# Kernel optimization log

Hardware: AMD Instinct MI355X
Metric: run time of the kernel (lower is better)

## Reference

```python
import jax, jax.numpy as jnp
import numpy as np

B, K = 2048, 256
ED = RD = HD = 256
AD = ED + RD          # action_dim = 512
IN = ED + HD + RD     # 768
NUM_E, NUM_R = 100000, 500
HUGE = jnp.float32(1e31)  # ops.HUGE_INT


def setup_inputs() -> dict:
    key = jax.random.key(0)
    ks = jax.random.split(key, 12)
    s = 0.05  # keep logits in a sane range
    E = jax.random.normal(ks[0], (B, ED), jnp.float32)
    H = jax.random.normal(ks[1], (B, HD), jnp.float32)
    Q = jax.random.normal(ks[2], (B, RD), jnp.float32)
    W1 = jax.random.normal(ks[3], (AD, IN), jnp.float32) * s
    b1 = jnp.zeros((AD,), jnp.float32)
    W2 = jax.random.normal(ks[4], (AD, AD), jnp.float32) * s
    b2 = jnp.zeros((AD,), jnp.float32)
    emb_r = jax.random.normal(ks[5], (NUM_R, RD), jnp.float32) * s
    emb_e = jax.random.normal(ks[6], (NUM_E, ED), jnp.float32) * s
    # binary action mask (variable-size action spaces, padded); col 0 always valid
    action_mask = (jax.random.uniform(ks[7], (B, K)) > 0.3).astype(jnp.float32)
    action_mask = action_mask.at[:, 0].set(1.0)
    r_space = jax.random.randint(ks[8], (B, K), 0, NUM_R)
    e_space = jax.random.randint(ks[9], (B, K), 0, NUM_E)
    return {"E": E, "H": H, "Q": Q, "W1": W1, "b1": b1, "W2": W2, "b2": b2,
            "emb_r": emb_r, "emb_e": emb_e, "action_mask": action_mask,
            "r_space": r_space, "e_space": e_space}


def reference(E, H, Q, W1, b1, W2, b2, emb_r, emb_e, action_mask, r_space, e_space):
    # state MLP: X = W2Dropout(W2(relu(W1(cat([E, H, Q])))))  (dropout = identity at eval)
    X = jnp.concatenate([E, H, Q], axis=-1)           # [B, IN]
    X = jax.nn.relu(X @ W1.T + b1)                    # [B, AD]
    X2 = X @ W2.T + b2                                # [B, AD]
    # gather action embeddings: A = cat([emb_r[r], emb_e[e]])  [B, K, AD]
    A = jnp.concatenate([emb_r[r_space], emb_e[e_space]], axis=-1)
    # masked softmax over action space
    scores = jnp.einsum('bkd,bd->bk', A, X2) - (1.0 - action_mask) * HUGE
    action_dist = jax.nn.softmax(scores, axis=-1)     # [B, K]
    entropy = -jnp.sum(action_dist * jnp.log(action_dist + 1e-20), axis=-1)  # [B]
    return action_dist, entropy
```

## Files before the change

kernel.cpp:

```cpp
#include <hip/hip_runtime.h>
#include <hip/hip_bf16.h>
#include <hip/hip_fp8.h>
#include <math.h>

#define B_   2048
#define K_   256
#define AD_  512
#define IN_  768
#define NR_  500
#define NRP_ 512
#define NE_  100000

typedef __attribute__((ext_vector_type(8))) short short8;
typedef __attribute__((ext_vector_type(4))) float float4v;
typedef __attribute__((ext_vector_type(4))) float f32x4;

__device__ __forceinline__ unsigned short f2bf(float f) {
    unsigned int u = __float_as_uint(f);
    unsigned int r = u + 0x7FFF + ((u >> 16) & 1);
    return (unsigned short)(r >> 16);
}
__device__ __forceinline__ float bf2f(short s) {
    return __uint_as_float(((unsigned int)(unsigned short)s) << 16);
}
__device__ __forceinline__ unsigned char f2fp8(float f) {
    __hip_fp8_e4m3 t(f);
    return (unsigned char)t.__x;
}
__device__ __forceinline__ float fp8tof(unsigned int byte) {
    __hip_fp8_e4m3 t; t.__x = (__hip_fp8_storage_t)byte; return (float)t;
}
__device__ __forceinline__ float dot4_fp8(unsigned int d, const float* x) {
    return fp8tof(d & 0xffu)         * x[0] + fp8tof((d >> 8) & 0xffu)  * x[1]
         + fp8tof((d >> 16) & 0xffu) * x[2] + fp8tof(d >> 24)           * x[3];
}

#define X_N4  (B_ * IN_ / 4)
#define W1_N4 (AD_ * IN_ / 4)
#define W2_N4 (AD_ * AD_ / 4)
#define ER_N4 (NR_ * 256 / 4)
#define PREPS_TOTAL (X_N4 + W1_N4 + W2_N4 + ER_N4)
__global__ __launch_bounds__(256) void prep_small_kernel(
    const float* __restrict__ E, const float* __restrict__ H,
    const float* __restrict__ Q, const float* __restrict__ W1,
    const float* __restrict__ W2, const float* __restrict__ emb_r,
    ushort* __restrict__ Xb, ushort* __restrict__ W1b,
    ushort* __restrict__ W2b, ushort* __restrict__ emb_rb)
{
    int t = blockIdx.x * 256 + threadIdx.x;
    const float* src; ushort* dst; long off;
    if (t < X_N4) {
        const int base = t * 4;
        const int row = base / IN_, col = base % IN_;
        src = (col < 256) ? &E[row * 256 + col]
            : (col < 512) ? &H[row * 256 + col - 256]
                          : &Q[row * 256 + col - 512];
        const float4 v = *(const float4*)src;
        ushort4 o;
        o.x = f2bf(v.x); o.y = f2bf(v.y); o.z = f2bf(v.z); o.w = f2bf(v.w);
        *(ushort4*)&Xb[base] = o;
        return;
    }
    t -= X_N4;
    if (t < W1_N4)                 { src = W1;    dst = W1b;    off = t; }
    else if (t < W1_N4 + W2_N4)    { src = W2;    dst = W2b;    off = t - W1_N4; }
    else if (t < W1_N4 + W2_N4 + ER_N4) { src = emb_r; dst = emb_rb; off = t - W1_N4 - W2_N4; }
    else return;
    const float4 v = *(const float4*)&src[off * 4];
    ushort4 o;
    o.x = f2bf(v.x); o.y = f2bf(v.y); o.z = f2bf(v.z); o.w = f2bf(v.w);
    *(ushort4*)&dst[off * 4] = o;
}

#define EE_N4 (NE_ * 256 / 4)
__device__ __forceinline__ void conv_range(
    const float* __restrict__ emb_e, unsigned char* __restrict__ emb_e8,
    int q0, int q1, int cb)
{
    const int stride = 256 * 256;
    const f32x4* __restrict__ src = (const f32x4*)emb_e;
    uchar4* __restrict__ dst = (uchar4*)emb_e8;
    int i = q0 + cb * 256 + (int)threadIdx.x;
    for (; i + 3 * stride < q1; i += 4 * stride) {
        f32x4 v0 = __builtin_nontemporal_load(src + i);
        f32x4 v1 = __builtin_nontemporal_load(src + i + stride);
        f32x4 v2 = __builtin_nontemporal_load(src + i + 2 * stride);
        f32x4 v3 = __builtin_nontemporal_load(src + i + 3 * stride);
        uchar4 o0, o1, o2, o3;
        o0.x = f2fp8(v0[0]); o0.y = f2fp8(v0[1]); o0.z = f2fp8(v0[2]); o0.w = f2fp8(v0[3]);
        o1.x = f2fp8(v1[0]); o1.y = f2fp8(v1[1]); o1.z = f2fp8(v1[2]); o1.w = f2fp8(v1[3]);
        o2.x = f2fp8(v2[0]); o2.y = f2fp8(v2[1]); o2.z = f2fp8(v2[2]); o2.w = f2fp8(v2[3]);
        o3.x = f2fp8(v3[0]); o3.y = f2fp8(v3[1]); o3.z = f2fp8(v3[2]); o3.w = f2fp8(v3[3]);
        dst[i] = o0; dst[i + stride] = o1; dst[i + 2 * stride] = o2; dst[i + 3 * stride] = o3;
    }
    for (; i < q1; i += stride) {
        f32x4 v = __builtin_nontemporal_load(src + i);
        uchar4 o;
        o.x = f2fp8(v[0]); o.y = f2fp8(v[1]); o.z = f2fp8(v[2]); o.w = f2fp8(v[3]);
        dst[i] = o;
    }
}

template<int K, bool RELU, bool OUT_BF16, bool BIAS, bool EMIT_RHALF>
__global__ __launch_bounds__(256) void gemm_bf16_kernel(
    const ushort* __restrict__ A, const ushort* __restrict__ Bw,
    const float* __restrict__ bias, ushort* __restrict__ outb,
    float* __restrict__ outf, ushort* __restrict__ rhalf,
    const float* __restrict__ emb_e, unsigned char* __restrict__ emb_e8,
    int q0, int q1)
{
    constexpr int PITCH = 72;
    __shared__ ushort Asl[2][64 * PITCH];
    __shared__ ushort Bsl[2][64 * PITCH];

    if (blockIdx.x >= 8) {
        conv_range(emb_e, emb_e8, q0, q1, (int)(blockIdx.x - 8) * 32 + (int)blockIdx.y);
        return;
    }

    const int tid = threadIdx.x;
    const int lane = tid & 63, w = tid >> 6;
    const int n0 = blockIdx.x * 64, m0 = blockIdx.y * 64;
    const int lrow = tid >> 2, lcg = (tid & 3) * 16;
    const int q = lane >> 4, l16 = lane & 15;

    const ushort* aptr = &A[(size_t)(m0 + lrow) * K + lcg];
    const ushort* bptr = &Bw[(size_t)(n0 + lrow) * K + lcg];

    short8 ra0 = *(const short8*)aptr;
    short8 ra1 = *(const short8*)(aptr + 8);
    short8 rb0 = *(const short8*)bptr;
    short8 rb1 = *(const short8*)(bptr + 8);
    *(short8*)&Asl[0][lrow * PITCH + lcg]     = ra0;
    *(short8*)&Asl[0][lrow * PITCH + lcg + 8] = ra1;
    *(short8*)&Bsl[0][lrow * PITCH + lcg]     = rb0;
    *(short8*)&Bsl[0][lrow * PITCH + lcg + 8] = rb1;

    float4v acc[4] = {};
    int buf = 0;
    __syncthreads();
    for (int k0 = 0; k0 < K; k0 += 64) {
        if (k0 + 64 < K) {
            ra0 = *(const short8*)(aptr + k0 + 64);
            ra1 = *(const short8*)(aptr + k0 + 64 + 8);
            rb0 = *(const short8*)(bptr + k0 + 64);
            rb1 = *(const short8*)(bptr + k0 + 64 + 8);
        }
        #pragma unroll
        for (int kh = 0; kh < 64; kh += 32) {
            const short8 af = *(const short8*)&Asl[buf][(w * 16 + l16) * PITCH + kh + q * 8];
            #pragma unroll
            for (int jn = 0; jn < 4; ++jn) {
                const short8 bfr = *(const short8*)&Bsl[buf][(jn * 16 + l16) * PITCH + kh + q * 8];
                acc[jn] = __builtin_amdgcn_mfma_f32_16x16x32_bf16(af, bfr, acc[jn], 0, 0, 0);
            }
        }
        if (k0 + 64 < K) {
            *(short8*)&Asl[buf ^ 1][lrow * PITCH + lcg]     = ra0;
            *(short8*)&Asl[buf ^ 1][lrow * PITCH + lcg + 8] = ra1;
            *(short8*)&Bsl[buf ^ 1][lrow * PITCH + lcg]     = rb0;
            *(short8*)&Bsl[buf ^ 1][lrow * PITCH + lcg + 8] = rb1;
            __syncthreads();
            buf ^= 1;
        }
    }
    #pragma unroll
    for (int jn = 0; jn < 4; ++jn) {
        const int n = n0 + jn * 16 + l16;
        const float bn = BIAS ? bias[n] : 0.0f;
        #pragma unroll
        for (int r = 0; r < 4; ++r) {
            const int m = m0 + w * 16 + q * 4 + r;
            float c = acc[jn][r] + bn;
            if (RELU) c = fmaxf(c, 0.0f);
            if (OUT_BF16) outb[(size_t)m * AD_ + n] = f2bf(c);
            else if (!EMIT_RHALF || n >= 256) outf[(size_t)m * AD_ + n] = c;
            if (EMIT_RHALF && n < 256) rhalf[(size_t)m * 256 + n] = f2bf(c);
        }
    }
}

__global__ __launch_bounds__(256) void scores_kernel(
    const float* __restrict__ X2, const float* __restrict__ R,
    const unsigned char* __restrict__ emb_e8, const float* __restrict__ mask,
    const int* __restrict__ r_space, const int* __restrict__ e_space,
    float* __restrict__ dist, float* __restrict__ entropy)
{
    const int b = blockIdx.x;
    const int tid = threadIdx.x;
    const int lane = tid & 63, wid = tid >> 6;
    const int l16 = lane & 15, q4 = lane >> 4;

    __shared__ int   s_e[K_];
    __shared__ float s_dot[K_];
    __shared__ float s_red[12];

    const int   e_mine = e_space[b * K_ + tid];
    const int   r_mine = r_space[b * K_ + tid];
    const float mk     = mask[b * K_ + tid];
    s_e[tid] = (mk != 0.0f) ? e_mine : 0;
    const float bias   = R[(size_t)b * NRP_ + r_mine] - (1.0f - mk) * 1e31f;
    float x[16];
    #pragma unroll
    for (int i = 0; i < 4; ++i) {
        const float4 xv = *(const float4*)&X2[(size_t)b * AD_ + 256 + l16 * 16 + i * 4];
        x[i * 4 + 0] = xv.x; x[i * 4 + 1] = xv.y;
        x[i * 4 + 2] = xv.z; x[i * 4 + 3] = xv.w;
    }
    __syncthreads();

    const int kbase = wid * 64;
    #pragma unroll
    for (int it = 0; it < 2; ++it) {
        uint4 wv[8];
        #pragma unroll
        for (int u = 0; u < 8; ++u) {
            const int row = kbase + it * 32 + u * 4 + q4;
            const int e = s_e[row];
            wv[u] = *(const uint4*)&emb_e8[(size_t)e * 256 + l16 * 16];
        }
        float p[8];
        #pragma unroll
        for (int u = 0; u < 8; ++u) {
            p[u] = dot4_fp8(wv[u].x, &x[0]) + dot4_fp8(wv[u].y, &x[4])
                 + dot4_fp8(wv[u].z, &x[8]) + dot4_fp8(wv[u].w, &x[12]);
        }
        #pragma unroll
        for (int off = 8; off >= 1; off >>= 1) {
            #pragma unroll
            for (int u = 0; u < 8; ++u) p[u] += __shfl_down(p[u], off, 16);
        }
        if (l16 == 0) {
            #pragma unroll
            for (int u = 0; u < 8; ++u) s_dot[kbase + it * 32 + u * 4 + q4] = p[u];
        }
    }
    __syncthreads();

    const float v = s_dot[tid] + bias;

    float m = v;
    #pragma unroll
    for (int off = 32; off >= 1; off >>= 1) m = fmaxf(m, __shfl_down(m, off));
    if (lane == 0) s_red[wid] = m;
    __syncthreads();
    if (tid == 0)
        s_red[8] = fmaxf(fmaxf(s_red[0], s_red[1]), fmaxf(s_red[2], s_red[3]));
    __syncthreads();
    const float bmax = s_red[8];

    const float ev = __expf(v - bmax);
    float s = ev;
    float t = ev * (v - bmax);
    #pragma unroll
    for (int off = 32; off >= 1; off >>= 1) {
        s += __shfl_down(s, off);
        t += __shfl_down(t, off);
    }
    if (lane == 0) { s_red[wid] = s; s_red[4 + wid] = t; }
    __syncthreads();
    if (tid == 0) {
        s_red[9]  = s_red[0] + s_red[1] + s_red[2] + s_red[3];
        s_red[10] = s_red[4] + s_red[5] + s_red[6] + s_red[7];
    }
    __syncthreads();
    const float ssum = s_red[9];

    dist[(size_t)b * K_ + tid] = ev / ssum;
    if (tid == 0)
        entropy[b] = logf(ssum) - s_red[10] / ssum;
}

extern "C" void kernel_launch(void* const* d_in, const int* in_sizes, int n_in,
                              void* d_out, int out_size, void* d_ws, size_t ws_size,
                              hipStream_t stream) {
    const float* E     = (const float*)d_in[0];
    const float* H     = (const float*)d_in[1];
    const float* Q     = (const float*)d_in[2];
    const float* W1    = (const float*)d_in[3];
    const float* b1    = (const float*)d_in[4];
    const float* W2    = (const float*)d_in[5];
    const float* b2    = (const float*)d_in[6];
    const float* emb_r = (const float*)d_in[7];
    const float* emb_e = (const float*)d_in[8];
    const float* mask  = (const float*)d_in[9];
    const int* r_space = (const int*)d_in[10];
    const int* e_space = (const int*)d_in[11];

    float* out_dist = (float*)d_out;
    float* out_ent  = out_dist + (size_t)B_ * K_;

    char* ws = (char*)d_ws;
    ushort* Xb     = (ushort*)ws;         ws += (size_t)B_ * IN_ * 2;
    ushort* W1b    = (ushort*)ws;         ws += (size_t)AD_ * IN_ * 2;
    ushort* W2b    = (ushort*)ws;         ws += (size_t)AD_ * AD_ * 2;
    ushort* emb_rb = (ushort*)ws;         ws += (size_t)NRP_ * 256 * 2;
    unsigned char* emb_e8 = (unsigned char*)ws; ws += (size_t)NE_ * 256;
    ushort* H1b    = (ushort*)ws;         ws += (size_t)B_ * AD_ * 2;
    float*  X2     = (float*)ws;          ws += (size_t)B_ * AD_ * 4;
    ushort* X2rb   = (ushort*)ws;         ws += (size_t)B_ * 256 * 2;
    float*  Rt     = (float*)ws;          ws += (size_t)B_ * NRP_ * 4;

    const int Q1 = 65536 * 40;
    const int Q2 = 65536 * 70;

    prep_small_kernel<<<(PREPS_TOTAL + 255) / 256, 256, 0, stream>>>(
        E, H, Q, W1, W2, emb_r, Xb, W1b, W2b, emb_rb);

    dim3 g(16, 32);
    gemm_bf16_kernel<IN_, true,  true,  true,  false><<<g, 256, 0, stream>>>(
        Xb, W1b, b1, H1b, nullptr, nullptr, emb_e, emb_e8, 0, Q1);
    gemm_bf16_kernel<AD_, false, false, true,  true ><<<g, 256, 0, stream>>>(
        H1b, W2b, b2, nullptr, X2, X2rb, emb_e, emb_e8, Q1, Q2);
    gemm_bf16_kernel<256, false, false, false, false><<<g, 256, 0, stream>>>(
        X2rb, emb_rb, nullptr, nullptr, Rt, nullptr, emb_e, emb_e8, Q2, EE_N4);

    scores_kernel<<<B_, 256, 0, stream>>>(X2, Rt, emb_e8, mask,
                                          r_space, e_space, out_dist, out_ent);
}
```

Measured before the change: 211.0 us.

## Fold emb_r projection into W2 and fuse bf16 conversion into GEMM loads

```diff
diff --git a/kernel.cpp b/kernel.cpp
--- a/kernel.cpp
+++ b/kernel.cpp
@@ -10,6 +10,7 @@
 #define NR_  500
 #define NRP_ 512
 #define NE_  100000
+#define PITCH 72
 
 typedef __attribute__((ext_vector_type(8))) short short8;
 typedef __attribute__((ext_vector_type(4))) float float4v;
@@ -20,9 +21,6 @@
     unsigned int r = u + 0x7FFF + ((u >> 16) & 1);
     return (unsigned short)(r >> 16);
 }
-__device__ __forceinline__ float bf2f(short s) {
-    return __uint_as_float(((unsigned int)(unsigned short)s) << 16);
-}
 __device__ __forceinline__ unsigned char f2fp8(float f) {
     __hip_fp8_e4m3 t(f);
     return (unsigned char)t.__x;
@@ -34,50 +32,21 @@
     return fp8tof(d & 0xffu)         * x[0] + fp8tof((d >> 8) & 0xffu)  * x[1]
          + fp8tof((d >> 16) & 0xffu) * x[2] + fp8tof(d >> 24)           * x[3];
 }
-
-#define X_N4  (B_ * IN_ / 4)
-#define W1_N4 (AD_ * IN_ / 4)
-#define W2_N4 (AD_ * AD_ / 4)
-#define ER_N4 (NR_ * 256 / 4)
-#define PREPS_TOTAL (X_N4 + W1_N4 + W2_N4 + ER_N4)
-__global__ __launch_bounds__(256) void prep_small_kernel(
-    const float* __restrict__ E, const float* __restrict__ H,
-    const float* __restrict__ Q, const float* __restrict__ W1,
-    const float* __restrict__ W2, const float* __restrict__ emb_r,
-    ushort* __restrict__ Xb, ushort* __restrict__ W1b,
-    ushort* __restrict__ W2b, ushort* __restrict__ emb_rb)
-{
-    int t = blockIdx.x * 256 + threadIdx.x;
-    const float* src; ushort* dst; long off;
-    if (t < X_N4) {
-        const int base = t * 4;
-        const int row = base / IN_, col = base % IN_;
-        src = (col < 256) ? &E[row * 256 + col]
-            : (col < 512) ? &H[row * 256 + col - 256]
-                          : &Q[row * 256 + col - 512];
-        const float4 v = *(const float4*)src;
-        ushort4 o;
-        o.x = f2bf(v.x); o.y = f2bf(v.y); o.z = f2bf(v.z); o.w = f2bf(v.w);
-        *(ushort4*)&Xb[base] = o;
-        return;
-    }
-    t -= X_N4;
-    if (t < W1_N4)                 { src = W1;    dst = W1b;    off = t; }
-    else if (t < W1_N4 + W2_N4)    { src = W2;    dst = W2b;    off = t - W1_N4; }
-    else if (t < W1_N4 + W2_N4 + ER_N4) { src = emb_r; dst = emb_rb; off = t - W1_N4 - W2_N4; }
-    else return;
-    const float4 v = *(const float4*)&src[off * 4];
-    ushort4 o;
-    o.x = f2bf(v.x); o.y = f2bf(v.y); o.z = f2bf(v.z); o.w = f2bf(v.w);
-    *(ushort4*)&dst[off * 4] = o;
+__device__ __forceinline__ short8 pack8(float4 a, float4 b) {
+    short8 r;
+    r[0] = (short)f2bf(a.x); r[1] = (short)f2bf(a.y);
+    r[2] = (short)f2bf(a.z); r[3] = (short)f2bf(a.w);
+    r[4] = (short)f2bf(b.x); r[5] = (short)f2bf(b.y);
+    r[6] = (short)f2bf(b.z); r[7] = (short)f2bf(b.w);
+    return r;
 }
 
 #define EE_N4 (NE_ * 256 / 4)
 __device__ __forceinline__ void conv_range(
     const float* __restrict__ emb_e, unsigned char* __restrict__ emb_e8,
-    int q0, int q1, int cb)
-{
-    const int stride = 256 * 256;
+    int q0, int q1, int cb, int nb)
+{
+    const int stride = nb * 256;
     const f32x4* __restrict__ src = (const f32x4*)emb_e;
     uchar4* __restrict__ dst = (uchar4*)emb_e8;
     int i = q0 + cb * 256 + (int)threadIdx.x;
@@ -101,65 +70,163 @@
     }
 }
 
-template<int K, bool RELU, bool OUT_BF16, bool BIAS, bool EMIT_RHALF>
-__global__ __launch_bounds__(256) void gemm_bf16_kernel(
-    const ushort* __restrict__ A, const ushort* __restrict__ Bw,
-    const float* __restrict__ bias, ushort* __restrict__ outb,
-    float* __restrict__ outf, ushort* __restrict__ rhalf,
+__device__ __forceinline__ void br_compute(
+    const float* __restrict__ emb_r, const float* __restrict__ b2,
+    float* __restrict__ br, int blk)
+{
+    const int tid = threadIdx.x;
+    const int rl = tid >> 3, sub = tid & 7;
+    const int r = blk * 32 + rl;
+    float acc = 0.0f;
+    if (r < NR_) {
+        const float4* er = (const float4*)&emb_r[(size_t)r * 256];
+        const float4* bb = (const float4*)b2;
+        #pragma unroll
+        for (int i = 0; i < 8; ++i) {
+            const float4 e = er[sub * 8 + i];
+            const float4 c = bb[sub * 8 + i];
+            acc += e.x * c.x + e.y * c.y + e.z * c.z + e.w * c.w;
+        }
+    }
+    #pragma unroll
+    for (int off = 4; off >= 1; off >>= 1) acc += __shfl_down(acc, off, 8);
+    if (sub == 0) br[r] = (r < NR_) ? acc : 0.0f;
+}
+
+__device__ __forceinline__ void mfma_step(
+    const ushort* __restrict__ Asb, const ushort* __restrict__ Bsb,
+    int w, int q, int l16, float4v acc[4])
+{
+    #pragma unroll
+    for (int kh = 0; kh < 64; kh += 32) {
+        const short8 af = *(const short8*)&Asb[(w * 16 + l16) * PITCH + kh + q * 8];
+        #pragma unroll
+        for (int jn = 0; jn < 4; ++jn) {
+            const short8 bfr = *(const short8*)&Bsb[(jn * 16 + l16) * PITCH + kh + q * 8];
+            acc[jn] = __builtin_amdgcn_mfma_f32_16x16x32_bf16(af, bfr, acc[jn], 0, 0, 0);
+        }
+    }
+}
+
+__device__ __forceinline__ const float* ehq_ptr(
+    const float* E, const float* H, const float* Q, int m, int k)
+{
+    return (k < 256) ? &E[(size_t)m * 256 + k]
+         : (k < 512) ? &H[(size_t)m * 256 + (k - 256)]
+                     : &Q[(size_t)m * 256 + (k - 512)];
+}
+__device__ __forceinline__ void ld_w2t(const float* __restrict__ W2, int col, int krow,
+                                       short8& lo, short8& hi)
+{
+    float v[16];
+    #pragma unroll
+    for (int i = 0; i < 16; ++i) v[i] = W2[(size_t)(krow + i) * 512 + col];
+    #pragma unroll
+    for (int i = 0; i < 8; ++i) { lo[i] = (short)f2bf(v[i]); hi[i] = (short)f2bf(v[8 + i]); }
+}
+__device__ __forceinline__ void ld_embr(const float* __restrict__ emb_r, int row, int k,
+                                        bool ok, short8& lo, short8& hi)
+{
+    if (ok) {
+        const float4* p = (const float4*)&emb_r[(size_t)row * 256 + k];
+        lo = pack8(p[0], p[1]); hi = pack8(p[2], p[3]);
+    } else {
+        #pragma unroll
+        for (int i = 0; i < 8; ++i) { lo[i] = 0; hi[i] = 0; }
+    }
+}
+
+__global__ __launch_bounds__(256) void k1_kernel(
+    const float* __restrict__ E, const float* __restrict__ H,
+    const float* __restrict__ Q, const float* __restrict__ W1,
+    const float* __restrict__ b1, const float* __restrict__ emb_r,
+    const float* __restrict__ b2, const float* __restrict__ W2,
+    ushort* __restrict__ H1b, ushort* __restrict__ W2Rb, float* __restrict__ br,
     const float* __restrict__ emb_e, unsigned char* __restrict__ emb_e8,
-    int q0, int q1)
-{
-    constexpr int PITCH = 72;
+    int q0, int q1, int nbconv)
+{
     __shared__ ushort Asl[2][64 * PITCH];
     __shared__ ushort Bsl[2][64 * PITCH];
-
-    if (blockIdx.x >= 8) {
-        conv_range(emb_e, emb_e8, q0, q1, (int)(blockIdx.x - 8) * 32 + (int)blockIdx.y);
-        return;
-    }
-
     const int tid = threadIdx.x;
     const int lane = tid & 63, w = tid >> 6;
+    const int q = lane >> 4, l16 = lane & 15;
+    const int lrow = tid >> 2, lcg = (tid & 3) * 16;
+
+    if (blockIdx.x >= 8) {
+        const int c = (int)(blockIdx.x - 8) * 32 + (int)blockIdx.y;
+        if (c >= 80) { conv_range(emb_e, emb_e8, q0, q1, c - 80, nbconv); return; }
+        if (c >= 64) { br_compute(emb_r, b2, br, c - 64); return; }
+        const int n0 = (c & 7) * 64, m0 = (c >> 3) * 64;
+        const int am = m0 + lrow;
+        const bool aok = am < NR_;
+        short8 pa0, pa1, pb0, pb1;
+        ld_embr(emb_r, am, lcg, aok, pa0, pa1);
+        ld_w2t(W2, n0 + lrow, lcg, pb0, pb1);
+        *(short8*)&Asl[0][lrow * PITCH + lcg]     = pa0;
+        *(short8*)&Asl[0][lrow * PITCH + lcg + 8] = pa1;
+        *(short8*)&Bsl[0][lrow * PITCH + lcg]     = pb0;
+        *(short8*)&Bsl[0][lrow * PITCH + lcg + 8] = pb1;
+        float4v acc[4] = {};
+        int buf = 0;
+        __syncthreads();
+        for (int k0 = 0; k0 < 256; k0 += 64) {
+            if (k0 + 64 < 256) {
+                ld_embr(emb_r, am, k0 + 64 + lcg, aok, pa0, pa1);
+                ld_w2t(W2, n0 + lrow, k0 + 64 + lcg, pb0, pb1);
+            }
+            mfma_step(&Asl[buf][0], &Bsl[buf][0], w, q, l16, acc);
+            if (k0 + 64 < 256) {
+                *(short8*)&Asl[buf ^ 1][lrow * PITCH + lcg]     = pa0;
+                *(short8*)&Asl[buf ^ 1][lrow * PITCH + lcg + 8] = pa1;
+                *(short8*)&Bsl[buf ^ 1][lrow * PITCH + lcg]     = pb0;
+                *(short8*)&Bsl[buf ^ 1][lrow * PITCH + lcg + 8] = pb1;
+                __syncthreads();
+                buf ^= 1;
+            }
+        }
+        #pragma unroll
+        for (int jn = 0; jn < 4; ++jn) {
+            const int n = n0 + jn * 16 + l16;
+            #pragma unroll
+            for (int r = 0; r < 4; ++r) {
+                const int m = m0 + w * 16 + q * 4 + r;
+                W2Rb[(size_t)m * 512 + n] = f2bf(acc[jn][r]);
+            }
+        }
+        return;
+    }
+
     const int n0 = blockIdx.x * 64, m0 = blockIdx.y * 64;
-    const int lrow = tid >> 2, lcg = (tid & 3) * 16;
-    const int q = lane >> 4, l16 = lane & 15;
-
-    const ushort* aptr = &A[(size_t)(m0 + lrow) * K + lcg];
-    const ushort* bptr = &Bw[(size_t)(n0 + lrow) * K + lcg];
-
-    short8 ra0 = *(const short8*)aptr;
-    short8 ra1 = *(const short8*)(aptr + 8);
-    short8 rb0 = *(const short8*)bptr;
-    short8 rb1 = *(const short8*)(bptr + 8);
-    *(short8*)&Asl[0][lrow * PITCH + lcg]     = ra0;
-    *(short8*)&Asl[0][lrow * PITCH + lcg + 8] = ra1;
-    *(short8*)&Bsl[0][lrow * PITCH + lcg]     = rb0;
-    *(short8*)&Bsl[0][lrow * PITCH + lcg + 8] = rb1;
-
+    const int am = m0 + lrow;
+    const float* w1p = &W1[(size_t)(n0 + lrow) * 768 + lcg];
+
+    short8 pa0, pa1, pb0, pb1;
+    {
+        const float4* ap = (const float4*)ehq_ptr(E, H, Q, am, lcg);
+        pa0 = pack8(ap[0], ap[1]); pa1 = pack8(ap[2], ap[3]);
+        const float4* bp = (const float4*)w1p;
+        pb0 = pack8(bp[0], bp[1]); pb1 = pack8(bp[2], bp[3]);
+    }
+    *(short8*)&Asl[0][lrow * PITCH + lcg]     = pa0;
+    *(short8*)&Asl[0][lrow * PITCH + lcg + 8] = pa1;
+    *(short8*)&Bsl[0][lrow * PITCH + lcg]     = pb0;
+    *(short8*)&Bsl[0][lrow * PITCH + lcg + 8] = pb1;
     float4v acc[4] = {};
     int buf = 0;
     __syncthreads();
-    for (int k0 = 0; k0 < K; k0 += 64) {
-        if (k0 + 64 < K) {
-            ra0 = *(const short8*)(aptr + k0 + 64);
-            ra1 = *(const short8*)(aptr + k0 + 64 + 8);
-            rb0 = *(const short8*)(bptr + k0 + 64);
-            rb1 = *(const short8*)(bptr + k0 + 64 + 8);
-        }
-        #pragma unroll
-        for (int kh = 0; kh < 64; kh += 32) {
-            const short8 af = *(const short8*)&Asl[buf][(w * 16 + l16) * PITCH + kh + q * 8];
-            #pragma unroll
-            for (int jn = 0; jn < 4; ++jn) {
-                const short8 bfr = *(const short8*)&Bsl[buf][(jn * 16 + l16) * PITCH + kh + q * 8];
-                acc[jn] = __builtin_amdgcn_mfma_f32_16x16x32_bf16(af, bfr, acc[jn], 0, 0, 0);
-            }
-        }
-        if (k0 + 64 < K) {
-            *(short8*)&Asl[buf ^ 1][lrow * PITCH + lcg]     = ra0;
-            *(short8*)&Asl[buf ^ 1][lrow * PITCH + lcg + 8] = ra1;
-            *(short8*)&Bsl[buf ^ 1][lrow * PITCH + lcg]     = rb0;
-            *(short8*)&Bsl[buf ^ 1][lrow * PITCH + lcg + 8] = rb1;
+    for (int k0 = 0; k0 < 768; k0 += 64) {
+        if (k0 + 64 < 768) {
+            const float4* ap = (const float4*)ehq_ptr(E, H, Q, am, k0 + 64 + lcg);
+            pa0 = pack8(ap[0], ap[1]); pa1 = pack8(ap[2], ap[3]);
+            const float4* bp = (const float4*)(w1p + k0 + 64);
+            pb0 = pack8(bp[0], bp[1]); pb1 = pack8(bp[2], bp[3]);
+        }
+        mfma_step(&Asl[buf][0], &Bsl[buf][0], w, q, l16, acc);
+        if (k0 + 64 < 768) {
+            *(short8*)&Asl[buf ^ 1][lrow * PITCH + lcg]     = pa0;
+            *(short8*)&Asl[buf ^ 1][lrow * PITCH + lcg + 8] = pa1;
+            *(short8*)&Bsl[buf ^ 1][lrow * PITCH + lcg]     = pb0;
+            *(short8*)&Bsl[buf ^ 1][lrow * PITCH + lcg + 8] = pb1;
             __syncthreads();
             buf ^= 1;
         }
@@ -167,21 +234,93 @@
     #pragma unroll
     for (int jn = 0; jn < 4; ++jn) {
         const int n = n0 + jn * 16 + l16;
-        const float bn = BIAS ? bias[n] : 0.0f;
+        const float bn = b1[n];
         #pragma unroll
         for (int r = 0; r < 4; ++r) {
             const int m = m0 + w * 16 + q * 4 + r;
-            float c = acc[jn][r] + bn;
-            if (RELU) c = fmaxf(c, 0.0f);
-            if (OUT_BF16) outb[(size_t)m * AD_ + n] = f2bf(c);
-            else if (!EMIT_RHALF || n >= 256) outf[(size_t)m * AD_ + n] = c;
-            if (EMIT_RHALF && n < 256) rhalf[(size_t)m * 256 + n] = f2bf(c);
+            H1b[(size_t)m * AD_ + n] = f2bf(fmaxf(acc[jn][r] + bn, 0.0f));
+        }
+    }
+}
+
+__global__ __launch_bounds__(256) void k2_kernel(
+    const ushort* __restrict__ H1b, const float* __restrict__ W2,
+    const ushort* __restrict__ W2Rb, const float* __restrict__ b2,
+    const float* __restrict__ br, float* __restrict__ X2e, float* __restrict__ Rt,
+    const float* __restrict__ emb_e, unsigned char* __restrict__ emb_e8,
+    int q0, int q1, int nbconv)
+{
+    __shared__ ushort Asl[2][64 * PITCH];
+    __shared__ ushort Bsl[2][64 * PITCH];
+    if (blockIdx.x >= 12) {
+        conv_range(emb_e, emb_e8, q0, q1,
+                   (int)(blockIdx.x - 12) * 32 + (int)blockIdx.y, nbconv);
+        return;
+    }
+    const int tid = threadIdx.x;
+    const int lane = tid & 63, w = tid >> 6;
+    const int q = lane >> 4, l16 = lane & 15;
+    const int lrow = tid >> 2, lcg = (tid & 3) * 16;
+    const bool isR = blockIdx.x >= 4;
+    const int n0 = isR ? (int)(blockIdx.x - 4) * 64 : (int)blockIdx.x * 64;
+    const int m0 = blockIdx.y * 64;
+
+    const ushort* aptr  = &H1b[(size_t)(m0 + lrow) * 512 + lcg];
+    const ushort* bptrR = &W2Rb[(size_t)(n0 + lrow) * 512 + lcg];
+    const float*  bptrW = &W2[(size_t)(256 + n0 + lrow) * 512 + lcg];
+
+    short8 pa0, pa1, pb0, pb1;
+    pa0 = *(const short8*)aptr; pa1 = *(const short8*)(aptr + 8);
+    if (isR) { pb0 = *(const short8*)bptrR; pb1 = *(const short8*)(bptrR + 8); }
+    else {
+        const float4* bp = (const float4*)bptrW;
+        pb0 = pack8(bp[0], bp[1]); pb1 = pack8(bp[2], bp[3]);
+    }
+    *(short8*)&Asl[0][lrow * PITCH + lcg]     = pa0;
+    *(short8*)&Asl[0][lrow * PITCH + lcg + 8] = pa1;
+    *(short8*)&Bsl[0][lrow * PITCH + lcg]     = pb0;
+    *(short8*)&Bsl[0][lrow * PITCH + lcg + 8] = pb1;
+    float4v acc[4] = {};
+    int buf = 0;
+    __syncthreads();
+    for (int k0 = 0; k0 < 512; k0 += 64) {
+        if (k0 + 64 < 512) {
+            pa0 = *(const short8*)(aptr + k0 + 64);
+            pa1 = *(const short8*)(aptr + k0 + 64 + 8);
+            if (isR) {
+                pb0 = *(const short8*)(bptrR + k0 + 64);
+                pb1 = *(const short8*)(bptrR + k0 + 64 + 8);
+            } else {
+                const float4* bp = (const float4*)(bptrW + k0 + 64);
+                pb0 = pack8(bp[0], bp[1]); pb1 = pack8(bp[2], bp[3]);
+            }
+        }
+        mfma_step(&Asl[buf][0], &Bsl[buf][0], w, q, l16, acc);
+        if (k0 + 64 < 512) {
+            *(short8*)&Asl[buf ^ 1][lrow * PITCH + lcg]     = pa0;
+            *(short8*)&Asl[buf ^ 1][lrow * PITCH + lcg + 8] = pa1;
+            *(short8*)&Bsl[buf ^ 1][lrow * PITCH + lcg]     = pb0;
+            *(short8*)&Bsl[buf ^ 1][lrow * PITCH + lcg + 8] = pb1;
+            __syncthreads();
+            buf ^= 1;
+        }
+    }
+    #pragma unroll
+    for (int jn = 0; jn < 4; ++jn) {
+        const int n = n0 + jn * 16 + l16;
+        const float bn = isR ? br[n] : b2[256 + n];
+        #pragma unroll
+        for (int r = 0; r < 4; ++r) {
+            const int m = m0 + w * 16 + q * 4 + r;
+            const float cv = acc[jn][r] + bn;
+            if (isR) Rt[(size_t)m * 512 + n] = cv;
+            else     X2e[(size_t)m * 256 + n] = cv;
         }
     }
 }
 
 __global__ __launch_bounds__(256) void scores_kernel(
-    const float* __restrict__ X2, const float* __restrict__ R,
+    const float* __restrict__ X2e, const float* __restrict__ R,
     const unsigned char* __restrict__ emb_e8, const float* __restrict__ mask,
     const int* __restrict__ r_space, const int* __restrict__ e_space,
     float* __restrict__ dist, float* __restrict__ entropy)
@@ -203,7 +342,7 @@
     float x[16];
     #pragma unroll
     for (int i = 0; i < 4; ++i) {
-        const float4 xv = *(const float4*)&X2[(size_t)b * AD_ + 256 + l16 * 16 + i * 4];
+        const float4 xv = *(const float4*)&X2e[(size_t)b * 256 + l16 * 16 + i * 4];
         x[i * 4 + 0] = xv.x; x[i * 4 + 1] = xv.y;
         x[i * 4 + 2] = xv.z; x[i * 4 + 3] = xv.w;
     }
@@ -291,30 +430,20 @@
     float* out_ent  = out_dist + (size_t)B_ * K_;
 
     char* ws = (char*)d_ws;
-    ushort* Xb     = (ushort*)ws;         ws += (size_t)B_ * IN_ * 2;
-    ushort* W1b    = (ushort*)ws;         ws += (size_t)AD_ * IN_ * 2;
-    ushort* W2b    = (ushort*)ws;         ws += (size_t)AD_ * AD_ * 2;
-    ushort* emb_rb = (ushort*)ws;         ws += (size_t)NRP_ * 256 * 2;
     unsigned char* emb_e8 = (unsigned char*)ws; ws += (size_t)NE_ * 256;
-    ushort* H1b    = (ushort*)ws;         ws += (size_t)B_ * AD_ * 2;
-    float*  X2     = (float*)ws;          ws += (size_t)B_ * AD_ * 4;
-    ushort* X2rb   = (ushort*)ws;         ws += (size_t)B_ * 256 * 2;
-    float*  Rt     = (float*)ws;          ws += (size_t)B_ * NRP_ * 4;
-
-    const int Q1 = 65536 * 40;
-    const int Q2 = 65536 * 70;
-
-    prep_small_kernel<<<(PREPS_TOTAL + 255) / 256, 256, 0, stream>>>(
-        E, H, Q, W1, W2, emb_r, Xb, W1b, W2b, emb_rb);
+    ushort* H1b  = (ushort*)ws;  ws += (size_t)B_ * AD_ * 2;
+    ushort* W2Rb = (ushort*)ws;  ws += (size_t)512 * 512 * 2;
+    float*  X2e  = (float*)ws;   ws += (size_t)B_ * 256 * 4;
+    float*  Rt   = (float*)ws;   ws += (size_t)B_ * NRP_ * 4;
+    float*  br   = (float*)ws;   ws += (size_t)NRP_ * 4;
+
+    const int Q1V = 3712000;
 
     dim3 g(16, 32);
-    gemm_bf16_kernel<IN_, true,  true,  true,  false><<<g, 256, 0, stream>>>(
-        Xb, W1b, b1, H1b, nullptr, nullptr, emb_e, emb_e8, 0, Q1);
-    gemm_bf16_kernel<AD_, false, false, true,  true ><<<g, 256, 0, stream>>>(
-        H1b, W2b, b2, nullptr, X2, X2rb, emb_e, emb_e8, Q1, Q2);
-    gemm_bf16_kernel<256, false, false, false, false><<<g, 256, 0, stream>>>(
-        X2rb, emb_rb, nullptr, nullptr, Rt, nullptr, emb_e, emb_e8, Q2, EE_N4);
-
-    scores_kernel<<<B_, 256, 0, stream>>>(X2, Rt, emb_e8, mask,
+    k1_kernel<<<g, 256, 0, stream>>>(E, H, Q, W1, b1, emb_r, b2, W2,
+                                     H1b, W2Rb, br, emb_e, emb_e8, 0, Q1V, 176);
+    k2_kernel<<<g, 256, 0, stream>>>(H1b, W2, W2Rb, b2, br, X2e, Rt,
+                                     emb_e, emb_e8, Q1V, EE_N4, 128);
+    scores_kernel<<<B_, 256, 0, stream>>>(X2e, Rt, emb_e8, mask,
                                           r_space, e_space, out_dist, out_ent);
 }
```

After: 214.6 us. No clear change (+1.7%).
